# Optimization experiments

Measured on AMD Instinct MI355X. Metric: run time of the kernel, lower is better.

## Reference

```python
import jax, jax.numpy as jnp
import numpy as np

N = 100000   # nodes
E = 1600000  # edges
F_IN = 256   # input features
H = 64       # hidden
C = 40       # classes


def setup_inputs() -> dict:
    key = jax.random.key(0)
    k = jax.random.split(key, 5)
    x = jax.random.normal(k[0], (N, F_IN), dtype=jnp.float32)
    edge_index = jax.random.randint(k[1], (2, E), 0, N, dtype=jnp.int64)
    edge_attr = jax.random.uniform(k[2], (E,), dtype=jnp.float32)
    # GCNConv params (glorot-ish scale), biases zero like reset_parameters
    W1 = jax.random.normal(k[3], (F_IN, H), dtype=jnp.float32) * (1.0 / np.sqrt(F_IN))
    b1 = jnp.zeros((H,), dtype=jnp.float32)
    W2 = jax.random.normal(k[4], (H, C), dtype=jnp.float32) * (1.0 / np.sqrt(H))
    b2 = jnp.zeros((C,), dtype=jnp.float32)
    return {"x": x, "edge_index": edge_index, "edge_attr": edge_attr,
            "W1": W1, "b1": b1, "W2": W2, "b2": b2}


def _gcn_conv(x, W, b, src, dst, norm):
    h = x @ W                                   # [N, out]
    msg = h[src] * norm[:, None]                # gather + edge scale [E+N, out]
    out = jax.ops.segment_sum(msg, dst, num_segments=N)
    return out + b


def reference(x, edge_index, edge_attr, W1, b1, W2, b2):
    # gcn_norm: add self-loops (weight 1), symmetric D^-1/2 A D^-1/2
    loop = jnp.arange(N, dtype=edge_index.dtype)
    src = jnp.concatenate([edge_index[0], loop])
    dst = jnp.concatenate([edge_index[1], loop])
    w = jnp.concatenate([edge_attr, jnp.ones((N,), dtype=edge_attr.dtype)])
    deg = jax.ops.segment_sum(w, dst, num_segments=N)
    dinv = jnp.where(deg > 0, jax.lax.rsqrt(jnp.maximum(deg, 1e-30)), 0.0)
    norm = dinv[src] * w * dinv[dst]

    h = _gcn_conv(x, W1, b1, src, dst, norm)
    h = jax.nn.relu(h)                          # dropout is identity in eval mode
    h = _gcn_conv(h, W2, b2, src, dst, norm)
    return jax.nn.log_softmax(h, axis=1)
```

## Files before the change

kernel.cpp:

```cpp
#include <hip/hip_runtime.h>
#include <math.h>

#define NN   100000
#define NE   1600000
#define FIN  256
#define HID  64
#define NC   40
#define NBKT 391
#define EPB  6250
#define CAP  4608

typedef __attribute__((ext_vector_type(8))) short short8;
typedef __attribute__((ext_vector_type(4))) float float4v;

static __device__ __forceinline__ short f2bf(float f) {
    unsigned u = __float_as_uint(f);
    u += 0x7FFFu + ((u >> 16) & 1u);
    return (short)(u >> 16);
}
static __device__ __forceinline__ float bf2f(unsigned short b) {
    return __uint_as_float((unsigned)b << 16);
}

__global__ __launch_bounds__(256) void w1cvt_k(const float* __restrict__ W1,
                                               short* __restrict__ w1t) {
    int t = blockIdx.x * 256 + threadIdx.x;
    int k = t >> 6, n = t & 63;
    w1t[n * FIN + k] = f2bf(W1[k * HID + n]);
}

__global__ __launch_bounds__(256) void phaseA_k(const int* __restrict__ src,
                                                const int* __restrict__ dst,
                                                const float* __restrict__ w,
                                                int* __restrict__ cursor,
                                                int2* __restrict__ bucketbuf) {
    __shared__ int  hist[NBKT];
    __shared__ int  sc[512];
    __shared__ int  loc_base[NBKT];
    __shared__ int  loc_cur[NBKT];
    __shared__ int  gb[NBKT];
    __shared__ int2 buf[EPB];
    const int t  = threadIdx.x;
    const int e0 = blockIdx.x * EPB;

    for (int i = t; i < NBKT; i += 256) hist[i] = 0;
    __syncthreads();
    for (int i = t; i < EPB; i += 256) atomicAdd(&hist[dst[e0 + i] >> 8], 1);
    __syncthreads();
    sc[t]       = (t       < NBKT) ? hist[t]       : 0;
    sc[t + 256] = (t + 256 < NBKT) ? hist[t + 256] : 0;
    __syncthreads();
    for (int off = 1; off < 512; off <<= 1) {
        int a0 = (t >= off) ? sc[t - off] : 0;
        int a1 = sc[t + 256 - off];
        __syncthreads();
        sc[t] += a0; sc[t + 256] += a1;
        __syncthreads();
    }
    for (int i = t; i < NBKT; i += 256) {
        int base = sc[i] - hist[i];
        loc_base[i] = base;
        loc_cur[i]  = base;
        gb[i] = atomicAdd(&cursor[i * 16], hist[i]);
    }
    __syncthreads();
    for (int i = t; i < EPB; i += 256) {
        int e = e0 + i;
        int d = dst[e];
        int b = d >> 8;
        int p = atomicAdd(&loc_cur[b], 1);
        buf[p] = make_int2(src[e] | ((d & 255) << 17), __float_as_int(w[e]));
    }
    __syncthreads();
    for (int b = t; b < NBKT; b += 256) {
        int lb = loc_base[b], n = hist[b];
        int2* dstp = bucketbuf + (size_t)b * CAP + gb[b];
        for (int i = 0; i < n; ++i) dstp[i] = buf[lb + i];
    }
}

__global__ __launch_bounds__(512) void scanB_k(const int* __restrict__ cursor,
                                               int* __restrict__ bucketbase,
                                               int* __restrict__ row_start) {
    __shared__ int tmp[512];
    int t = threadIdx.x;
    int v = (t < NBKT) ? cursor[t * 16] : 0;
    tmp[t] = v;
    __syncthreads();
    for (int off = 1; off < 512; off <<= 1) {
        int add = (t >= off) ? tmp[t - off] : 0;
        __syncthreads(); tmp[t] += add; __syncthreads();
    }
    if (t < NBKT) bucketbase[t] = tmp[t] - v;
    if (t == 0) { bucketbase[NBKT] = NE; row_start[NN] = NE; }
}

__global__ __launch_bounds__(256) void phaseB_k(const int* __restrict__ bucketbase,
                                                const int2* __restrict__ bucketbuf,
                                                int2* __restrict__ e8,
                                                int* __restrict__ row_start,
                                                float* __restrict__ dinv) {
    __shared__ int2 buf[CAP];
    __shared__ int2 buf2[CAP];
    __shared__ int  hist2[256];
    __shared__ int  tmp[256];
    __shared__ int  base2[257];
    __shared__ int  cur2[256];
    const int b = blockIdx.x, t = threadIdx.x;
    const int g0   = bucketbase[b];
    const int cntb = bucketbase[b + 1] - g0;
    const int n0   = b * 256;
    const int nnb  = (NN - n0 < 256) ? (NN - n0) : 256;

    hist2[t] = 0;
    __syncthreads();
    const int2* bb = bucketbuf + (size_t)b * CAP;
    for (int i = t; i < cntb; i += 256) {
        int2 kv = bb[i];
        buf[i] = kv;
        atomicAdd(&hist2[kv.x >> 17], 1);
    }
    __syncthreads();
    int v = hist2[t];
    tmp[t] = v;
    __syncthreads();
    for (int off = 1; off < 256; off <<= 1) {
        int add = (t >= off) ? tmp[t - off] : 0;
        __syncthreads(); tmp[t] += add; __syncthreads();
    }
    int excl = tmp[t] - v;
    base2[t] = excl;
    cur2[t]  = excl;
    if (t == 0) base2[256] = cntb;
    if (t < nnb) row_start[n0 + t] = g0 + excl;
    __syncthreads();
    for (int i = t; i < cntb; i += 256) {
        int2 kv = buf[i];
        int d = kv.x >> 17;
        int p = atomicAdd(&cur2[d], 1);
        buf2[p] = make_int2(kv.x & 0x1FFFF, kv.y);
    }
    __syncthreads();
    for (int i = t; i < cntb; i += 256) e8[g0 + i] = buf2[i];
    if (t < nnb) {
        float s = 0.f;
        int j1 = base2[t + 1];
        for (int j = base2[t]; j < j1; ++j) s += __int_as_float(buf2[j].y);
        dinv[n0 + t] = rsqrtf(1.0f + s);
    }
}

__global__ __launch_bounds__(256) void gemm1_mfma_k(const float* __restrict__ x,
                                                    const short* __restrict__ w1t,
                                                    const float* __restrict__ dinv,
                                                    unsigned short* __restrict__ h1) {
    const int wave = threadIdx.x >> 6;
    const int lane = threadIdx.x & 63;
    const int m    = lane & 15;
    const int quad = lane >> 4;
    const int r0   = blockIdx.x * 64 + wave * 16;
    const int row  = r0 + m;
    const int rcl  = (row < NN) ? row : (NN - 1);
    const float* xrow = x + (size_t)rcl * FIN + quad * 8;

    float4 xv[16];
#pragma unroll
    for (int kc = 0; kc < 8; ++kc) {
        xv[2 * kc]     = *(const float4*)(xrow + kc * 32);
        xv[2 * kc + 1] = *(const float4*)(xrow + kc * 32 + 4);
    }

    float4v acc0 = {0.f,0.f,0.f,0.f}, acc1 = acc0, acc2 = acc0, acc3 = acc0;

#pragma unroll
    for (int kc = 0; kc < 8; ++kc) {
        const int kof = kc * 32 + quad * 8;
        float4 xa = xv[2 * kc];
        float4 xb = xv[2 * kc + 1];
        short8 a;
        a[0] = f2bf(xa.x); a[1] = f2bf(xa.y); a[2] = f2bf(xa.z); a[3] = f2bf(xa.w);
        a[4] = f2bf(xb.x); a[5] = f2bf(xb.y); a[6] = f2bf(xb.z); a[7] = f2bf(xb.w);
        short8 b0 = *(const short8*)(w1t + (0 * 16 + m) * FIN + kof);
        short8 b1 = *(const short8*)(w1t + (1 * 16 + m) * FIN + kof);
        short8 b2 = *(const short8*)(w1t + (2 * 16 + m) * FIN + kof);
        short8 b3 = *(const short8*)(w1t + (3 * 16 + m) * FIN + kof);
        acc0 = __builtin_amdgcn_mfma_f32_16x16x32_bf16(a, b0, acc0, 0, 0, 0);
        acc1 = __builtin_amdgcn_mfma_f32_16x16x32_bf16(a, b1, acc1, 0, 0, 0);
        acc2 = __builtin_amdgcn_mfma_f32_16x16x32_bf16(a, b2, acc2, 0, 0, 0);
        acc3 = __builtin_amdgcn_mfma_f32_16x16x32_bf16(a, b3, acc3, 0, 0, 0);
    }
#pragma unroll
    for (int r = 0; r < 4; ++r) {
        int rr = r0 + quad * 4 + r;
        if (rr < NN) {
            float dv = dinv[rr];
            unsigned short* hp = h1 + (size_t)rr * HID + m;
            hp[0]  = (unsigned short)f2bf(acc0[r] * dv);
            hp[16] = (unsigned short)f2bf(acc1[r] * dv);
            hp[32] = (unsigned short)f2bf(acc2[r] * dv);
            hp[48] = (unsigned short)f2bf(acc3[r] * dv);
        }
    }
}

__global__ __launch_bounds__(256) void gatherA_k(const int* __restrict__ row_start,
                                                 const int2* __restrict__ e8,
                                                 const float* __restrict__ dinv,
                                                 const unsigned short* __restrict__ h,
                                                 const float* __restrict__ b1,
                                                 unsigned short* __restrict__ Rp) {
    const int v    = blockIdx.x * 4 + (threadIdx.x >> 6);
    const int lane = threadIdx.x & 63;
    const int half = lane >> 5;
    const int fp2  = (lane & 31) << 1;
    const int i0 = row_start[v], i1 = row_start[v + 1];

    float a0 = 0.f, a1 = 0.f, c0 = 0.f, c1 = 0.f;
    int i = i0 + half;
    for (; i + 2 < i1; i += 4) {
        int2 ea = e8[i];
        int2 eb = e8[i + 2];
        unsigned pa = *(const unsigned*)(h + (size_t)ea.x * HID + fp2);
        unsigned pb = *(const unsigned*)(h + (size_t)eb.x * HID + fp2);
        float wa = __int_as_float(ea.y), wb = __int_as_float(eb.y);
        a0 = fmaf(__uint_as_float(pa << 16),          wa, a0);
        a1 = fmaf(__uint_as_float(pa & 0xFFFF0000u), wa, a1);
        c0 = fmaf(__uint_as_float(pb << 16),          wb, c0);
        c1 = fmaf(__uint_as_float(pb & 0xFFFF0000u), wb, c1);
    }
    if (i < i1) {
        int2 ea = e8[i];
        unsigned pa = *(const unsigned*)(h + (size_t)ea.x * HID + fp2);
        float wa = __int_as_float(ea.y);
        a0 = fmaf(__uint_as_float(pa << 16),          wa, a0);
        a1 = fmaf(__uint_as_float(pa & 0xFFFF0000u), wa, a1);
    }
    a0 += c0; a1 += c1;
    a0 += __shfl_xor(a0, 32);
    a1 += __shfl_xor(a1, 32);

    const float dv = dinv[v];
    unsigned ps = *(const unsigned*)(h + (size_t)v * HID + fp2);
    float r0 = dv * (a0 + __uint_as_float(ps << 16));
    float r1 = dv * (a1 + __uint_as_float(ps & 0xFFFF0000u));
    r0 = fmaxf(r0 + b1[fp2],     0.f);
    r1 = fmaxf(r1 + b1[fp2 + 1], 0.f);
    if (half == 0) {
        unsigned pk = (unsigned)(unsigned short)f2bf(dv * r0)
                    | ((unsigned)(unsigned short)f2bf(dv * r1) << 16);
        *(unsigned*)(Rp + (size_t)v * HID + fp2) = pk;
    }
}

__global__ __launch_bounds__(256) void gatherB_k(const int* __restrict__ row_start,
                                                 const int2* __restrict__ e8,
                                                 const float* __restrict__ dinv,
                                                 const unsigned short* __restrict__ Rp,
                                                 float* __restrict__ agg2) {
    const int v    = blockIdx.x * 4 + (threadIdx.x >> 6);
    const int lane = threadIdx.x & 63;
    const int half = lane >> 5;
    const int fp2  = (lane & 31) << 1;
    const int i0 = row_start[v], i1 = row_start[v + 1];

    float a0 = 0.f, a1 = 0.f, c0 = 0.f, c1 = 0.f;
    int i = i0 + half;
    for (; i + 2 < i1; i += 4) {
        int2 ea = e8[i];
        int2 eb = e8[i + 2];
        unsigned pa = *(const unsigned*)(Rp + (size_t)ea.x * HID + fp2);
        unsigned pb = *(const unsigned*)(Rp + (size_t)eb.x * HID + fp2);
        float wa = __int_as_float(ea.y), wb = __int_as_float(eb.y);
        a0 = fmaf(__uint_as_float(pa << 16),          wa, a0);
        a1 = fmaf(__uint_as_float(pa & 0xFFFF0000u), wa, a1);
        c0 = fmaf(__uint_as_float(pb << 16),          wb, c0);
        c1 = fmaf(__uint_as_float(pb & 0xFFFF0000u), wb, c1);
    }
    if (i < i1) {
        int2 ea = e8[i];
        unsigned pa = *(const unsigned*)(Rp + (size_t)ea.x * HID + fp2);
        float wa = __int_as_float(ea.y);
        a0 = fmaf(__uint_as_float(pa << 16),          wa, a0);
        a1 = fmaf(__uint_as_float(pa & 0xFFFF0000u), wa, a1);
    }
    a0 += c0; a1 += c1;
    a0 += __shfl_xor(a0, 32);
    a1 += __shfl_xor(a1, 32);

    const float dv = dinv[v];
    unsigned ps = *(const unsigned*)(Rp + (size_t)v * HID + fp2);
    float r0 = dv * (a0 + __uint_as_float(ps << 16));
    float r1 = dv * (a1 + __uint_as_float(ps & 0xFFFF0000u));
    if (half == 0)
        *(float2*)(agg2 + (size_t)v * HID + fp2) = make_float2(r0, r1);
}

__global__ __launch_bounds__(256) void gemm3_logsm_k(const float* __restrict__ agg2,
                                                     const float* __restrict__ W2,
                                                     const float* __restrict__ b2,
                                                     float* __restrict__ out) {
    __shared__ float w2s[HID * NC];
    __shared__ float b2s[NC];
    for (int i = threadIdx.x; i < HID * NC; i += 256) w2s[i] = W2[i];
    if (threadIdx.x < NC) b2s[threadIdx.x] = b2[threadIdx.x];
    __syncthreads();

    const int r = blockIdx.x * 256 + threadIdx.x;
    if (r >= NN) return;
    float acc[NC];
#pragma unroll
    for (int c = 0; c < NC; ++c) acc[c] = b2s[c];

    const float4* row4 = (const float4*)(agg2 + (size_t)r * HID);
    for (int kk = 0; kk < HID; kk += 4) {
        float4 v = row4[kk >> 2];
#pragma unroll
        for (int c = 0; c < NC; ++c) {
            acc[c] = fmaf(v.x, w2s[(kk + 0) * NC + c], acc[c]);
            acc[c] = fmaf(v.y, w2s[(kk + 1) * NC + c], acc[c]);
            acc[c] = fmaf(v.z, w2s[(kk + 2) * NC + c], acc[c]);
            acc[c] = fmaf(v.w, w2s[(kk + 3) * NC + c], acc[c]);
        }
    }
    float m = acc[0];
#pragma unroll
    for (int c = 1; c < NC; ++c) m = fmaxf(m, acc[c]);
    float s = 0.f;
#pragma unroll
    for (int c = 0; c < NC; ++c) s += __expf(acc[c] - m);
    float lg = m + __logf(s);
    float* outp = out + (size_t)r * NC;
#pragma unroll
    for (int c = 0; c < NC; c += 4)
        *(float4*)&outp[c] = make_float4(acc[c] - lg, acc[c+1] - lg, acc[c+2] - lg, acc[c+3] - lg);
}

extern "C" void kernel_launch(void* const* d_in, const int* in_sizes, int n_in,
                              void* d_out, int out_size, void* d_ws, size_t ws_size,
                              hipStream_t stream) {
    const float* x  = (const float*)d_in[0];
    const int*   ei = (const int*)d_in[1];
    const float* ea = (const float*)d_in[2];
    const float* W1 = (const float*)d_in[3];
    const float* b1 = (const float*)d_in[4];
    const float* W2 = (const float*)d_in[5];
    const float* b2 = (const float*)d_in[6];
    const int* src = ei;
    const int* dst = ei + NE;
    float* out = (float*)d_out;

    char* ws = (char*)d_ws;
    float* dinv       = (float*)(ws + 0);
    int*   row_start  = (int*)  (ws + 400000);
    int*   cursor     = (int*)  (ws + 800016);
    int*   bucketbase = (int*)  (ws + 825040);
    int2*  e8         = (int2*) (ws + 826608);
    unsigned short* h1 = (unsigned short*)(ws + 13626608);
    unsigned short* Rp = (unsigned short*)(ws + 26426608);
    float* agg2       = (float*)(ws + 39226608);
    short* w1t        = (short*)(ws + 64826608);
    int2*  bucketbuf  = (int2*)agg2;

    hipMemsetAsync(cursor, 0, 391 * 16 * sizeof(int), stream);

    w1cvt_k <<<64,   256, 0, stream>>>(W1, w1t);
    phaseA_k<<<256,  256, 0, stream>>>(src, dst, ea, cursor, bucketbuf);
    scanB_k <<<1,    512, 0, stream>>>(cursor, bucketbase, row_start);
    phaseB_k<<<NBKT, 256, 0, stream>>>(bucketbase, bucketbuf, e8, row_start, dinv);

    gemm1_mfma_k <<<(NN + 63) / 64, 256, 0, stream>>>(x, w1t, dinv, h1);
    gatherA_k    <<<NN / 4, 256, 0, stream>>>(row_start, e8, dinv, h1, b1, Rp);
    gatherB_k    <<<NN / 4, 256, 0, stream>>>(row_start, e8, dinv, Rp, agg2);
    gemm3_logsm_k<<<(NN + 255) / 256, 256, 0, stream>>>(agg2, W2, b2, out);
}
```

Measured before the change: 411.1 us.

## Gather neighbor rows with 16-byte loads across 8 edge slots per wave

Both CSR gather kernels now map each wave to 8 edge slots of 8 lanes, with each lane loading 8 bf16 features as a uint4, so each wave handles 16 edges per iteration instead of 4. This cuts the number of load instructions per edge and raises memory-level parallelism for the random row gathers. The cost is a 3-stage cross-lane shuffle reduction over 8 accumulators, plus wasted lanes on low-degree nodes because inactive slots fall back to a dummy row. A compiler memory barrier is also added after the x loads in the first GEMM to pin load scheduling.

```diff
diff --git a/kernel.cpp b/kernel.cpp
--- a/kernel.cpp
+++ b/kernel.cpp
@@ -169,6 +169,7 @@
         xv[2 * kc]     = *(const float4*)(xrow + kc * 32);
         xv[2 * kc + 1] = *(const float4*)(xrow + kc * 32 + 4);
     }
+    asm volatile("" ::: "memory");
 
     float4v acc0 = {0.f,0.f,0.f,0.f}, acc1 = acc0, acc2 = acc0, acc3 = acc0;
 
@@ -211,44 +212,64 @@
                                                  unsigned short* __restrict__ Rp) {
     const int v    = blockIdx.x * 4 + (threadIdx.x >> 6);
     const int lane = threadIdx.x & 63;
-    const int half = lane >> 5;
-    const int fp2  = (lane & 31) << 1;
+    const int slot = lane >> 3;
+    const int fg   = lane & 7;
     const int i0 = row_start[v], i1 = row_start[v + 1];
 
-    float a0 = 0.f, a1 = 0.f, c0 = 0.f, c1 = 0.f;
-    int i = i0 + half;
-    for (; i + 2 < i1; i += 4) {
-        int2 ea = e8[i];
-        int2 eb = e8[i + 2];
-        unsigned pa = *(const unsigned*)(h + (size_t)ea.x * HID + fp2);
-        unsigned pb = *(const unsigned*)(h + (size_t)eb.x * HID + fp2);
-        float wa = __int_as_float(ea.y), wb = __int_as_float(eb.y);
-        a0 = fmaf(__uint_as_float(pa << 16),          wa, a0);
-        a1 = fmaf(__uint_as_float(pa & 0xFFFF0000u), wa, a1);
-        c0 = fmaf(__uint_as_float(pb << 16),          wb, c0);
-        c1 = fmaf(__uint_as_float(pb & 0xFFFF0000u), wb, c1);
-    }
-    if (i < i1) {
-        int2 ea = e8[i];
-        unsigned pa = *(const unsigned*)(h + (size_t)ea.x * HID + fp2);
-        float wa = __int_as_float(ea.y);
-        a0 = fmaf(__uint_as_float(pa << 16),          wa, a0);
-        a1 = fmaf(__uint_as_float(pa & 0xFFFF0000u), wa, a1);
-    }
-    a0 += c0; a1 += c1;
-    a0 += __shfl_xor(a0, 32);
-    a1 += __shfl_xor(a1, 32);
+    float acc[8] = {0.f,0.f,0.f,0.f,0.f,0.f,0.f,0.f};
+    for (int i = i0; i < i1; i += 16) {
+        int iiA = i + slot, iiB = i + 8 + slot;
+        bool okA = iiA < i1, okB = iiB < i1;
+        int2 eA = e8[okA ? iiA : (NE - 1)];
+        int2 eB = e8[okB ? iiB : (NE - 1)];
+        int  sA = okA ? eA.x : 0;
+        int  sB = okB ? eB.x : 0;
+        float wA = okA ? __int_as_float(eA.y) : 0.f;
+        float wB = okB ? __int_as_float(eB.y) : 0.f;
+        uint4 pA = *(const uint4*)(h + (size_t)sA * HID + fg * 8);
+        uint4 pB = *(const uint4*)(h + (size_t)sB * HID + fg * 8);
+        acc[0] = fmaf(__uint_as_float(pA.x << 16),         wA, acc[0]);
+        acc[1] = fmaf(__uint_as_float(pA.x & 0xFFFF0000u), wA, acc[1]);
+        acc[2] = fmaf(__uint_as_float(pA.y << 16),         wA, acc[2]);
+        acc[3] = fmaf(__uint_as_float(pA.y & 0xFFFF0000u), wA, acc[3]);
+        acc[4] = fmaf(__uint_as_float(pA.z << 16),         wA, acc[4]);
+        acc[5] = fmaf(__uint_as_float(pA.z & 0xFFFF0000u), wA, acc[5]);
+        acc[6] = fmaf(__uint_as_float(pA.w << 16),         wA, acc[6]);
+        acc[7] = fmaf(__uint_as_float(pA.w & 0xFFFF0000u), wA, acc[7]);
+        acc[0] = fmaf(__uint_as_float(pB.x << 16),         wB, acc[0]);
+        acc[1] = fmaf(__uint_as_float(pB.x & 0xFFFF0000u), wB, acc[1]);
+        acc[2] = fmaf(__uint_as_float(pB.y << 16),         wB, acc[2]);
+        acc[3] = fmaf(__uint_as_float(pB.y & 0xFFFF0000u), wB, acc[3]);
+        acc[4] = fmaf(__uint_as_float(pB.z << 16),         wB, acc[4]);
+        acc[5] = fmaf(__uint_as_float(pB.z & 0xFFFF0000u), wB, acc[5]);
+        acc[6] = fmaf(__uint_as_float(pB.w << 16),         wB, acc[6]);
+        acc[7] = fmaf(__uint_as_float(pB.w & 0xFFFF0000u), wB, acc[7]);
+    }
+#pragma unroll
+    for (int mk = 8; mk <= 32; mk <<= 1) {
+#pragma unroll
+        for (int q = 0; q < 8; ++q) acc[q] += __shfl_xor(acc[q], mk);
+    }
 
     const float dv = dinv[v];
-    unsigned ps = *(const unsigned*)(h + (size_t)v * HID + fp2);
-    float r0 = dv * (a0 + __uint_as_float(ps << 16));
-    float r1 = dv * (a1 + __uint_as_float(ps & 0xFFFF0000u));
-    r0 = fmaxf(r0 + b1[fp2],     0.f);
-    r1 = fmaxf(r1 + b1[fp2 + 1], 0.f);
-    if (half == 0) {
-        unsigned pk = (unsigned)(unsigned short)f2bf(dv * r0)
-                    | ((unsigned)(unsigned short)f2bf(dv * r1) << 16);
-        *(unsigned*)(Rp + (size_t)v * HID + fp2) = pk;
+    uint4 ps = *(const uint4*)(h + (size_t)v * HID + fg * 8);
+    float4 bA = *(const float4*)(b1 + fg * 8);
+    float4 bB = *(const float4*)(b1 + fg * 8 + 4);
+    float r0 = fmaxf(dv * (acc[0] + __uint_as_float(ps.x << 16))         + bA.x, 0.f);
+    float r1 = fmaxf(dv * (acc[1] + __uint_as_float(ps.x & 0xFFFF0000u)) + bA.y, 0.f);
+    float r2 = fmaxf(dv * (acc[2] + __uint_as_float(ps.y << 16))         + bA.z, 0.f);
+    float r3 = fmaxf(dv * (acc[3] + __uint_as_float(ps.y & 0xFFFF0000u)) + bA.w, 0.f);
+    float r4 = fmaxf(dv * (acc[4] + __uint_as_float(ps.z << 16))         + bB.x, 0.f);
+    float r5 = fmaxf(dv * (acc[5] + __uint_as_float(ps.z & 0xFFFF0000u)) + bB.y, 0.f);
+    float r6 = fmaxf(dv * (acc[6] + __uint_as_float(ps.w << 16))         + bB.z, 0.f);
+    float r7 = fmaxf(dv * (acc[7] + __uint_as_float(ps.w & 0xFFFF0000u)) + bB.w, 0.f);
+    if (slot == 0) {
+        uint4 pk;
+        pk.x = (unsigned)(unsigned short)f2bf(dv * r0) | ((unsigned)(unsigned short)f2bf(dv * r1) << 16);
+        pk.y = (unsigned)(unsigned short)f2bf(dv * r2) | ((unsigned)(unsigned short)f2bf(dv * r3) << 16);
+        pk.z = (unsigned)(unsigned short)f2bf(dv * r4) | ((unsigned)(unsigned short)f2bf(dv * r5) << 16);
+        pk.w = (unsigned)(unsigned short)f2bf(dv * r6) | ((unsigned)(unsigned short)f2bf(dv * r7) << 16);
+        *(uint4*)(Rp + (size_t)v * HID + fg * 8) = pk;
     }
 }
 
@@ -259,40 +280,60 @@
                                                  float* __restrict__ agg2) {
     const int v    = blockIdx.x * 4 + (threadIdx.x >> 6);
     const int lane = threadIdx.x & 63;
-    const int half = lane >> 5;
-    const int fp2  = (lane & 31) << 1;
+    const int slot = lane >> 3;
+    const int fg   = lane & 7;
     const int i0 = row_start[v], i1 = row_start[v + 1];
 
-    float a0 = 0.f, a1 = 0.f, c0 = 0.f, c1 = 0.f;
-    int i = i0 + half;
-    for (; i + 2 < i1; i += 4) {
-        int2 ea = e8[i];
-        int2 eb = e8[i + 2];
-        unsigned pa = *(const unsigned*)(Rp + (size_t)ea.x * HID + fp2);
-        unsigned pb = *(const unsigned*)(Rp + (size_t)eb.x * HID + fp2);
-        float wa = __int_as_float(ea.y), wb = __int_as_float(eb.y);
-        a0 = fmaf(__uint_as_float(pa << 16),          wa, a0);
-        a1 = fmaf(__uint_as_float(pa & 0xFFFF0000u), wa, a1);
-        c0 = fmaf(__uint_as_float(pb << 16),          wb, c0);
-        c1 = fmaf(__uint_as_float(pb & 0xFFFF0000u), wb, c1);
-    }
-    if (i < i1) {
-        int2 ea = e8[i];
-        unsigned pa = *(const unsigned*)(Rp + (size_t)ea.x * HID + fp2);
-        float wa = __int_as_float(ea.y);
-        a0 = fmaf(__uint_as_float(pa << 16),          wa, a0);
-        a1 = fmaf(__uint_as_float(pa & 0xFFFF0000u), wa, a1);
-    }
-    a0 += c0; a1 += c1;
-    a0 += __shfl_xor(a0, 32);
-    a1 += __shfl_xor(a1, 32);
+    float acc[8] = {0.f,0.f,0.f,0.f,0.f,0.f,0.f,0.f};
+    for (int i = i0; i < i1; i += 16) {
+        int iiA = i + slot, iiB = i + 8 + slot;
+        bool okA = iiA < i1, okB = iiB < i1;
+        int2 eA = e8[okA ? iiA : (NE - 1)];
+        int2 eB = e8[okB ? iiB : (NE - 1)];
+        int  sA = okA ? eA.x : 0;
+        int  sB = okB ? eB.x : 0;
+        float wA = okA ? __int_as_float(eA.y) : 0.f;
+        float wB = okB ? __int_as_float(eB.y) : 0.f;
+        uint4 pA = *(const uint4*)(Rp + (size_t)sA * HID + fg * 8);
+        uint4 pB = *(const uint4*)(Rp + (size_t)sB * HID + fg * 8);
+        acc[0] = fmaf(__uint_as_float(pA.x << 16),         wA, acc[0]);
+        acc[1] = fmaf(__uint_as_float(pA.x & 0xFFFF0000u), wA, acc[1]);
+        acc[2] = fmaf(__uint_as_float(pA.y << 16),         wA, acc[2]);
+        acc[3] = fmaf(__uint_as_float(pA.y & 0xFFFF0000u), wA, acc[3]);
+        acc[4] = fmaf(__uint_as_float(pA.z << 16),         wA, acc[4]);
+        acc[5] = fmaf(__uint_as_float(pA.z & 0xFFFF0000u), wA, acc[5]);
+        acc[6] = fmaf(__uint_as_float(pA.w << 16),         wA, acc[6]);
+        acc[7] = fmaf(__uint_as_float(pA.w & 0xFFFF0000u), wA, acc[7]);
+        acc[0] = fmaf(__uint_as_float(pB.x << 16),         wB, acc[0]);
+        acc[1] = fmaf(__uint_as_float(pB.x & 0xFFFF0000u), wB, acc[1]);
+        acc[2] = fmaf(__uint_as_float(pB.y << 16),         wB, acc[2]);
+        acc[3] = fmaf(__uint_as_float(pB.y & 0xFFFF0000u), wB, acc[3]);
+        acc[4] = fmaf(__uint_as_float(pB.z << 16),         wB, acc[4]);
+        acc[5] = fmaf(__uint_as_float(pB.z & 0xFFFF0000u), wB, acc[5]);
+        acc[6] = fmaf(__uint_as_float(pB.w << 16),         wB, acc[6]);
+        acc[7] = fmaf(__uint_as_float(pB.w & 0xFFFF0000u), wB, acc[7]);
+    }
+#pragma unroll
+    for (int mk = 8; mk <= 32; mk <<= 1) {
+#pragma unroll
+        for (int q = 0; q < 8; ++q) acc[q] += __shfl_xor(acc[q], mk);
+    }
 
     const float dv = dinv[v];
-    unsigned ps = *(const unsigned*)(Rp + (size_t)v * HID + fp2);
-    float r0 = dv * (a0 + __uint_as_float(ps << 16));
-    float r1 = dv * (a1 + __uint_as_float(ps & 0xFFFF0000u));
-    if (half == 0)
-        *(float2*)(agg2 + (size_t)v * HID + fp2) = make_float2(r0, r1);
+    uint4 ps = *(const uint4*)(Rp + (size_t)v * HID + fg * 8);
+    if (slot == 0) {
+        float4 oA, oB;
+        oA.x = dv * (acc[0] + __uint_as_float(ps.x << 16));
+        oA.y = dv * (acc[1] + __uint_as_float(ps.x & 0xFFFF0000u));
+        oA.z = dv * (acc[2] + __uint_as_float(ps.y << 16));
+        oA.w = dv * (acc[3] + __uint_as_float(ps.y & 0xFFFF0000u));
+        oB.x = dv * (acc[4] + __uint_as_float(ps.z << 16));
+        oB.y = dv * (acc[5] + __uint_as_float(ps.z & 0xFFFF0000u));
+        oB.z = dv * (acc[6] + __uint_as_float(ps.w << 16));
+        oB.w = dv * (acc[7] + __uint_as_float(ps.w & 0xFFFF0000u));
+        *(float4*)(agg2 + (size_t)v * HID + fg * 8)     = oA;
+        *(float4*)(agg2 + (size_t)v * HID + fg * 8 + 4) = oB;
+    }
 }
 
 __global__ __launch_bounds__(256) void gemm3_logsm_k(const float* __restrict__ agg2,
```

Result: faster. 379.3 us (-7.7%).
